# Kernel optimization log

Hardware: AMD Instinct MI355X
Metric: run time of the kernel (lower is better)

The kernel has to match this reference:

```python
import jax, jax.numpy as jnp
import numpy as np

B, T, E, NH, NLEV = 16, 2048, 1024, 16, 12
HD = E // NH


def _level_matrix(length):
    # Vectorized version of get_level_index_weak (base=2): levels[t, s] for s < t.
    tt, ss = np.meshgrid(np.arange(length), np.arange(length), indexing='ij')
    t = tt.copy(); s = ss.copy()
    lev = np.zeros((length, length), dtype=np.int32)
    active = tt > ss
    while active.any():
        l = np.floor(np.log2(np.maximum(t, 1))).astype(np.int64)
        v = (1 << l)
        done = active & (s < v)
        lev[done] = (l[done] + 1).astype(np.int32)
        cont = active & ~done
        t = np.where(cont, t - v, t)
        s = np.where(cont, s - v, s)
        active = cont
    return lev  # lev[t,t] = 0 (diagonal uses level 0)


def setup_inputs() -> dict:
    key = jax.random.key(0)
    ks = jax.random.split(key, 12)
    s = 0.02
    inp = {
        'x': jax.random.normal(ks[0], (B, T, E), jnp.float32),
        'Wq': jax.random.normal(ks[1], (E, E), jnp.float32) * s,
        'bq': jnp.zeros((E,), jnp.float32),
        'Wk': jax.random.normal(ks[2], (E, E), jnp.float32) * s,
        'bk': jnp.zeros((E,), jnp.float32),
        'Wv': jax.random.normal(ks[3], (E, E), jnp.float32) * s,
        'bv': jnp.zeros((E,), jnp.float32),
        'A_log': jax.random.normal(ks[4], (T, NH), jnp.float32),
        'A_bias': jnp.zeros((T, NH), jnp.float32),
        'L': jax.random.normal(ks[5], (T, NH, NLEV), jnp.float32),
        'L_bias': jnp.zeros((T, NH, NLEV), jnp.float32),
        'Wo': jax.random.normal(ks[6], (E, E), jnp.float32) * s,
        'bo': jnp.zeros((E,), jnp.float32),
        'levels': jnp.asarray(_level_matrix(T)),
    }
    return inp


def reference(x, Wq, bq, Wk, bk, Wv, bv, A_log, A_bias, L, L_bias, Wo, bo, levels):
    Bn, Tn, En = x.shape
    NHh = A_log.shape[1]
    HDd = En // NHh
    # q/k projections exist in the original forward but are never used by the
    # hierarchical attention; keep only v (q/k are dead code -> omitted).
    v = (x @ Wv.T + bv).reshape(Bn, Tn, NHh, HDd).transpose(0, 2, 1, 3)  # [B,H,T,D]

    # Decay factors: prod(A[s+1:t+1]) == exp(cumsum(logA)[t] - cumsum(logA)[s]).
    A = jax.nn.sigmoid(A_log + A_bias)            # [T, H]
    cs = jnp.cumsum(jnp.log(A), axis=0)           # [T, H]
    decay = jnp.exp(cs[:, None, :] - cs[None, :, :])  # [t, s, H]; diag == 1

    # Hierarchical level weights: G[t, s, h] = (L + L_bias)[t, h, levels[t, s]].
    Le = L + L_bias                               # [T, H, NLEV]
    G = Le[jnp.arange(Tn)[:, None], :, levels]    # [t, s, H]

    causal = jnp.tril(jnp.ones((Tn, Tn), dtype=bool))[:, :, None]
    Hm = jnp.where(causal, G * decay, jnp.zeros((), x.dtype))  # [t, s, H]

    # Original softmaxes the full row (upper triangle is 0, not -inf) -> keep that.
    attn = jax.nn.softmax(Hm, axis=1)             # over source dim s
    out = jnp.einsum('tsh,bhsd->bhtd', attn, v)   # [B,H,T,D]
    out = out.transpose(0, 2, 1, 3).reshape(Bn, Tn, En)
    return out @ Wo.T + bo
```

## Files before the change

kernel.cpp:

```cpp
#include <hip/hip_runtime.h>
#include <stdint.h>

static constexpr int Bn = 16, Tn = 2048, En = 1024, NHn = 16, HDn = 64, NLEVn = 12;

typedef __attribute__((ext_vector_type(8))) short short8;
typedef __attribute__((ext_vector_type(4))) float floatx4;

__device__ __forceinline__ unsigned short f2bf(float f) {
  unsigned int u = __float_as_uint(f);
  u += 0x7fffu + ((u >> 16) & 1u);
  return (unsigned short)(u >> 16);
}
__device__ __forceinline__ float bf2f(unsigned short s) {
  return __uint_as_float(((unsigned int)s) << 16);
}

__device__ __forceinline__ void async16(const unsigned short* g, unsigned short* l) {
  __builtin_amdgcn_global_load_lds(
      (const __attribute__((address_space(1))) unsigned int*)g,
      (__attribute__((address_space(3))) unsigned int*)l, 16, 0, 0);
}

__global__ void k_cvt(const float* __restrict__ in, unsigned short* __restrict__ out, int n4) {
  int i = blockIdx.x * 256 + threadIdx.x;
  if (i < n4) {
    float4 v = ((const float4*)in)[i];
    ushort4 o;
    o.x = f2bf(v.x); o.y = f2bf(v.y); o.z = f2bf(v.z); o.w = f2bf(v.w);
    ((ushort4*)out)[i] = o;
  }
}

__global__ void k_scan(const float* __restrict__ A_log, const float* __restrict__ A_bias,
                       float* __restrict__ csT) {
  int h = blockIdx.x;
  int tid = threadIdx.x;
  __shared__ float part[256];
  float loc[8];
  float run = 0.f;
#pragma unroll
  for (int j = 0; j < 8; j++) {
    int t = tid * 8 + j;
    float x = A_log[t * NHn + h] + A_bias[t * NHn + h];
    float ls = -log1pf(__expf(-x));
    run += ls;
    loc[j] = run;
  }
  part[tid] = run;
  __syncthreads();
  for (int d = 1; d < 256; d <<= 1) {
    float v = (tid >= d) ? part[tid - d] : 0.f;
    __syncthreads();
    part[tid] += v;
    __syncthreads();
  }
  float off = (tid > 0) ? part[tid - 1] : 0.f;
#pragma unroll
  for (int j = 0; j < 8; j++) csT[(size_t)h * Tn + tid * 8 + j] = loc[j] + off;
}

__global__ void k_weights(const float* __restrict__ L, const float* __restrict__ Lb,
                          const int* __restrict__ levels, const float* __restrict__ csT,
                          unsigned short* __restrict__ P, float* __restrict__ denom) {
  int t = blockIdx.x;
  int tid = threadIdx.x;
  __shared__ float Lrow[NHn * NLEVn];
  __shared__ float cst[NHn];
  __shared__ float dsum[NHn];
  if (tid < NHn * NLEVn) Lrow[tid] = L[t * NHn * NLEVn + tid] + Lb[t * NHn * NLEVn + tid];
  if (tid < NHn) { cst[tid] = csT[(size_t)tid * Tn + t]; dsum[tid] = 0.f; }
  __syncthreads();
  float acc[NHn];
#pragma unroll
  for (int h = 0; h < NHn; h++) acc[h] = 0.f;
  for (int s = tid; s < Tn; s += 256) {
    int lev = levels[(size_t)t * Tn + s];
    bool causal = (s <= t);
#pragma unroll
    for (int h = 0; h < NHn; h++) {
      float w = 1.f;
      if (causal) {
        float csr = csT[(size_t)h * Tn + s];
        float dec = __expf(cst[h] - csr);
        w = __expf(Lrow[h * NLEVn + lev] * dec);
      }
      unsigned short pb = f2bf(w);
      acc[h] += bf2f(pb);
      P[((size_t)h * Tn + t) * Tn + s] = pb;
    }
  }
  int lane = tid & 63;
#pragma unroll
  for (int h = 0; h < NHn; h++) {
    float v = acc[h];
    for (int o = 32; o > 0; o >>= 1) v += __shfl_down(v, o, 64);
    if (lane == 0) atomicAdd(&dsum[h], v);
  }
  __syncthreads();
  if (tid < NHn) denom[(size_t)tid * Tn + t] = dsum[tid];
}

__global__ __launch_bounds__(512)
void k_gemm_v(const unsigned short* __restrict__ A, const unsigned short* __restrict__ Bm,
              const float* __restrict__ bias, unsigned short* __restrict__ vt) {
  __shared__ unsigned short smem[24576];
  unsigned short* As = smem;
  unsigned short* Bs = smem + 16384;
  const int K = 1024;
  int tid = threadIdx.x;
  int wave = tid >> 6, lane = tid & 63;
  int wm = wave >> 1, wn = wave & 1;

  int flat = blockIdx.y * 8 + blockIdx.x;
  int xcd = flat & 7, slot = flat >> 3;
  int strip = xcd * 16 + (slot >> 3);
  int nt = slot & 7;
  int bm = strip * 256, bn = nt * 128;

  floatx4 zero4 = {0.f, 0.f, 0.f, 0.f};
  floatx4 acc[4][4];
#pragma unroll
  for (int i = 0; i < 4; i++)
#pragma unroll
    for (int j = 0; j < 4; j++) acc[i][j] = zero4;

  for (int k0 = 0; k0 < K; k0 += 64) {
    __syncthreads();
#pragma unroll
    for (int j = 0; j < 4; j++) {
      int f = j * 512 + tid;
      int r = f >> 3, c = f & 7;
      int cg = c ^ (r & 7);
      async16(&A[(size_t)(bm + r) * K + k0 + cg * 8], &As[f * 8]);
    }
#pragma unroll
    for (int j = 0; j < 2; j++) {
      int f = j * 512 + tid;
      int r = f >> 3, c = f & 7;
      int cg = c ^ (r & 7);
      async16(&Bm[(size_t)(bn + r) * K + k0 + cg * 8], &Bs[f * 8]);
    }
    __syncthreads();
#pragma unroll
    for (int kk = 0; kk < 2; kk++) {
      short8 af[4], bfr[4];
      int cgk = kk * 4 + (lane >> 4);
#pragma unroll
      for (int i = 0; i < 4; i++) {
        int m = wm * 64 + i * 16 + (lane & 15);
        af[i] = *(const short8*)&As[m * 64 + ((cgk ^ (m & 7)) * 8)];
        int n = wn * 64 + i * 16 + (lane & 15);
        bfr[i] = *(const short8*)&Bs[n * 64 + ((cgk ^ (n & 7)) * 8)];
      }
#pragma unroll
      for (int i = 0; i < 4; i++)
#pragma unroll
        for (int j = 0; j < 4; j++)
          acc[i][j] = __builtin_amdgcn_mfma_f32_16x16x32_bf16(af[i], bfr[j], acc[i][j], 0, 0, 0);
    }
  }

  int b = bm >> 11, t0 = bm & 2047;
  unsigned short* Ct = smem;
  const int S = 264;
#pragma unroll 1
  for (int pass = 0; pass < 2; pass++) {
    __syncthreads();
    if (wn == pass) {
#pragma unroll
      for (int i = 0; i < 4; i++) {
#pragma unroll
        for (int j = 0; j < 4; j++) {
          int colL = j * 16 + (lane & 15);
          float bia = bias[bn + pass * 64 + colL];
          int rowb = wm * 64 + i * 16 + (lane >> 4) * 4;
          ushort4 p;
          p.x = f2bf(acc[i][j][0] + bia);
          p.y = f2bf(acc[i][j][1] + bia);
          p.z = f2bf(acc[i][j][2] + bia);
          p.w = f2bf(acc[i][j][3] + bia);
          *(ushort4*)&Ct[colL * S + rowb] = p;
        }
      }
    }
    __syncthreads();
#pragma unroll
    for (int cc = 0; cc < 4; cc++) {
      int colL = wave * 8 + cc * 2 + (lane >> 5);
      int gc = bn + pass * 64 + colL;
      int h = gc >> 6, d = gc & 63;
      int tt = (lane & 31) * 8;
      short8 v = *(const short8*)&Ct[colL * S + tt];
      *(short8*)&vt[((size_t)((h * Bn + b) * HDn + d)) * Tn + t0 + tt] = v;
    }
  }
}


#define STAGE_A(kt, half, buf)                                                   \
  {                                                                              \
    _Pragma("unroll")                                                            \
    for (int j_ = 0; j_ < 2; j_++) {                                             \
      int f_ = j_ * 512 + tid;                                                   \
      int r_ = f_ >> 3, c_ = f_ & 7;                                             \
      int cg_ = c_ ^ (r_ & 7);                                                   \
      async16(&Ap[(size_t)(bm + (half) * 128 + r_) * K + (kt) * 64 + cg_ * 8],   \
              &smem[(buf) * 32768 + ((half) * 128 + r_) * 64 + c_ * 8]);         \
    }                                                                            \
  }

#define STAGE_B(kt, half, buf)                                                   \
  {                                                                              \
    _Pragma("unroll")                                                            \
    for (int j_ = 0; j_ < 2; j_++) {                                             \
      int f_ = j_ * 512 + tid;                                                   \
      int r_ = f_ >> 3, c_ = f_ & 7;                                             \
      int cg_ = c_ ^ (r_ & 7);                                                   \
      async16(&Bp[(size_t)(bn + (half) * 128 + r_) * K + (kt) * 64 + cg_ * 8],   \
              &smem[(buf) * 32768 + 16384 + ((half) * 128 + r_) * 64 + c_ * 8]); \
    }                                                                            \
  }

#define LOAD_A(buf, Mh)                                                          \
  {                                                                              \
    _Pragma("unroll")                                                            \
    for (int ii_ = 0; ii_ < 4; ii_++) {                                          \
      int m_ = (Mh) * 128 + wm * 64 + ii_ * 16 + (lane & 15);                    \
      _Pragma("unroll")                                                          \
      for (int kk_ = 0; kk_ < 2; kk_++) {                                        \
        int cgk_ = kk_ * 4 + (lane >> 4);                                        \
        aR[ii_][kk_] =                                                           \
            *(const short8*)&smem[(buf) * 32768 + m_ * 64 + ((cgk_ ^ (m_ & 7)) * 8)]; \
      }                                                                          \
    }                                                                            \
  }

#define LOAD_B(buf, Nh)                                                          \
  {                                                                              \
    _Pragma("unroll")                                                            \
    for (int jj_ = 0; jj_ < 2; jj_++) {                                          \
      int n_ = (Nh) * 128 + wn * 32 + jj_ * 16 + (lane & 15);                    \
      _Pragma("unroll")                                                          \
      for (int kk_ = 0; kk_ < 2; kk_++) {                                        \
        int cgk_ = kk_ * 4 + (lane >> 4);                                        \
        bR[jj_][kk_] = *(const short8*)&smem[(buf) * 32768 + 16384 + n_ * 64 +   \
                                             ((cgk_ ^ (n_ & 7)) * 8)];           \
      }                                                                          \
    }                                                                            \
  }

#define MFMA16(Mh, Nh)                                                           \
  {                                                                              \
    __builtin_amdgcn_s_setprio(1);                                               \
    _Pragma("unroll")                                                            \
    for (int kk_ = 0; kk_ < 2; kk_++)                                            \
      _Pragma("unroll")                                                          \
      for (int ii_ = 0; ii_ < 4; ii_++)                                          \
        _Pragma("unroll")                                                        \
        for (int jj_ = 0; jj_ < 2; jj_++)                                        \
          acc[(Mh) * 4 + ii_][(Nh) * 2 + jj_] = __builtin_amdgcn_mfma_f32_16x16x32_bf16( \
              aR[ii_][kk_], bR[jj_][kk_], acc[(Mh) * 4 + ii_][(Nh) * 2 + jj_], 0, 0, 0); \
    __builtin_amdgcn_s_setprio(0);                                               \
  }

#define WAIT6 asm volatile("s_waitcnt vmcnt(6)" ::: "memory")
#define BAR                                                                      \
  {                                                                              \
    asm volatile("" ::: "memory");                                               \
    __builtin_amdgcn_s_barrier();                                                \
    asm volatile("" ::: "memory");                                               \
  }

#define KTILE_BODY(buf, nbuf, tn)                                                \
  {                                                                              \
                                  \
    STAGE_A(tn, 0, nbuf);                                                        \
    WAIT6; BAR;                                                                  \
    LOAD_A(buf, 0);                                                              \
    LOAD_B(buf, 0);                                                              \
    MFMA16(0, 0);                                                                \
    BAR;                                                                         \
                               \
    STAGE_B(tn, 0, nbuf);                                                        \
    WAIT6; BAR;                                                                  \
    LOAD_B(buf, 1);                                                              \
    MFMA16(0, 1);                                                                \
    BAR;                                                                         \
                               \
    STAGE_B(tn, 1, nbuf);                                                        \
    WAIT6; BAR;                                                                  \
    LOAD_A(buf, 1);                                                              \
    MFMA16(1, 1);                                                                \
    BAR;                                                                         \
                            \
    STAGE_A(tn, 1, nbuf);                                                        \
    WAIT6; BAR;                                                                  \
    LOAD_B(buf, 0);                                                              \
    MFMA16(1, 0);                                                                \
    BAR;                                                                         \
  }

__global__ __launch_bounds__(512, 2)
void k_gemm_attn(const unsigned short* __restrict__ P, const unsigned short* __restrict__ vt,
                 const float* __restrict__ denom, unsigned short* __restrict__ outp) {
  __shared__ unsigned short smem[65536];
  const int K = Tn;
  int tid = threadIdx.x;
  int wave = tid >> 6, lane = tid & 63;
  int wm = wave >> 2, wn = wave & 3;

  int flat = blockIdx.y * 8 + blockIdx.x;
  int wg = (flat & 7) * 64 + (flat >> 3);
  int h = wg >> 5;
  int mt = (wg >> 2) & 7, nt = wg & 3;
  int bm = mt * 256, bn = nt * 256;

  const unsigned short* Ap = P + (size_t)h * Tn * Tn;
  const unsigned short* Bp = vt + (size_t)h * (Bn * HDn) * Tn;

  floatx4 zero4 = {0.f, 0.f, 0.f, 0.f};
  floatx4 acc[8][4];
#pragma unroll
  for (int i = 0; i < 8; i++)
#pragma unroll
    for (int j = 0; j < 4; j++) acc[i][j] = zero4;

  short8 aR[4][2], bR[2][2];

  STAGE_A(0, 0, 0);
  STAGE_B(0, 0, 0);
  STAGE_B(0, 1, 0);
  STAGE_A(0, 1, 0);

  const int nk = K / 64;
  for (int t = 0; t < nk; t++) {
    int buf = t & 1, nbuf = buf ^ 1;
    int tn = (t < nk - 1) ? t + 1 : nk - 1;
    KTILE_BODY(buf, nbuf, tn);
  }
  asm volatile("s_waitcnt vmcnt(0)" ::: "memory");

#pragma unroll
  for (int i = 0; i < 8; i++) {
    int rb = bm + (i >> 2) * 128 + wm * 64 + (i & 3) * 16 + (lane >> 4) * 4;
#pragma unroll
    for (int r = 0; r < 4; r++) {
      int row = rb + r;
      float sc = 1.f / denom[(size_t)h * Tn + row];
#pragma unroll
      for (int j = 0; j < 4; j++) {
        int col = bn + (j >> 1) * 128 + wn * 32 + (j & 1) * 16 + (lane & 15);
        int b = col >> 6, d = col & 63;
        outp[((size_t)(b * Tn + row)) * En + h * HDn + d] = f2bf(acc[i][j][r] * sc);
      }
    }
  }
}

__global__ __launch_bounds__(512, 2)
void k_gemm_out(const unsigned short* __restrict__ A, const unsigned short* __restrict__ Bm,
                const float* __restrict__ bias, float* __restrict__ out) {
  __shared__ unsigned short smem[65536];
  const int K = 1024, N = 1024;
  int tid = threadIdx.x;
  int wave = tid >> 6, lane = tid & 63;
  int wm = wave >> 2, wn = wave & 3;

  int flat = blockIdx.y * 8 + blockIdx.x;
  int wg = (flat & 7) * 64 + (flat >> 3);
  int mt = wg >> 2, nt = wg & 3;
  int bm = mt * 256, bn = nt * 256;

  const unsigned short* Ap = A;
  const unsigned short* Bp = Bm;

  floatx4 zero4 = {0.f, 0.f, 0.f, 0.f};
  floatx4 acc[8][4];
#pragma unroll
  for (int i = 0; i < 8; i++)
#pragma unroll
    for (int j = 0; j < 4; j++) acc[i][j] = zero4;

  short8 aR[4][2], bR[2][2];

  STAGE_A(0, 0, 0);
  STAGE_B(0, 0, 0);
  STAGE_B(0, 1, 0);
  STAGE_A(0, 1, 0);

  const int nk = K / 64;
  for (int t = 0; t < nk; t++) {
    int buf = t & 1, nbuf = buf ^ 1;
    int tn = (t < nk - 1) ? t + 1 : nk - 1;
    KTILE_BODY(buf, nbuf, tn);
  }
  asm volatile("s_waitcnt vmcnt(0)" ::: "memory");

#pragma unroll
  for (int i = 0; i < 8; i++) {
    int rb = bm + (i >> 2) * 128 + wm * 64 + (i & 3) * 16 + (lane >> 4) * 4;
#pragma unroll
    for (int r = 0; r < 4; r++) {
      int row = rb + r;
#pragma unroll
      for (int j = 0; j < 4; j++) {
        int col = bn + (j >> 1) * 128 + wn * 32 + (j & 1) * 16 + (lane & 15);
        out[(size_t)row * N + col] = acc[i][j][r] + bias[col];
      }
    }
  }
}

extern "C" void kernel_launch(void* const* d_in, const int* in_sizes, int n_in,
                              void* d_out, int out_size, void* d_ws, size_t ws_size,
                              hipStream_t stream) {
  const float* x      = (const float*)d_in[0];
  const float* Wv     = (const float*)d_in[5];
  const float* bv     = (const float*)d_in[6];
  const float* A_log  = (const float*)d_in[7];
  const float* A_bias = (const float*)d_in[8];
  const float* L      = (const float*)d_in[9];
  const float* Lb     = (const float*)d_in[10];
  const float* Wo     = (const float*)d_in[11];
  const float* bo     = (const float*)d_in[12];
  const int* levels   = (const int*)d_in[13];
  float* out = (float*)d_out;

  char* ws = (char*)d_ws;
  float* csT           = (float*)(ws + 0);
  float* denom         = (float*)(ws + 131072);
  unsigned short* Wvb  = (unsigned short*)(ws + 262144);
  unsigned short* Wob  = (unsigned short*)(ws + 2359296);
  unsigned short* xb   = (unsigned short*)(ws + 4456448);
  unsigned short* Pw   = (unsigned short*)(ws + 4456448);
  unsigned short* vt   = (unsigned short*)(ws + 138674176);
  unsigned short* outp = (unsigned short*)(ws + 205783040);
  if (ws_size < 272891904ULL) return;

  int nx4 = Bn * Tn * En / 4;
  k_cvt<<<(nx4 + 255) / 256, 256, 0, stream>>>(x, xb, nx4);
  int nw4 = En * En / 4;
  k_cvt<<<(nw4 + 255) / 256, 256, 0, stream>>>(Wv, Wvb, nw4);
  k_cvt<<<(nw4 + 255) / 256, 256, 0, stream>>>(Wo, Wob, nw4);
  k_scan<<<NHn, 256, 0, stream>>>(A_log, A_bias, csT);

  k_gemm_v<<<dim3(8, 128), 512, 0, stream>>>(xb, Wvb, bv, vt);

  k_weights<<<Tn, 256, 0, stream>>>(L, Lb, levels, csT, Pw, denom);

  k_gemm_attn<<<dim3(8, 64), 512, 0, stream>>>(Pw, vt, denom, outp);

  k_gemm_out<<<dim3(8, 64), 512, 0, stream>>>(outp, Wob, bo, out);
}
```

Before: 606.3 us.

## Skip upper-triangle blocks in attention GEMM using precomputed V tail sums

Past the causal diagonal every attention weight is exp(0)=1, so the weights kernel now writes only up to the 256-aligned block boundary and adds the constant tail count to the denominator. A new kernel precomputes suffix sums of V over 256-row blocks, and the attention GEMM runs K only up to its row tile, then adds the tail sum before normalising. This roughly halves the P writes and the attention GEMM work, at the cost of an extra small kernel. The tail sums are kept in scratch space at the end of the output buffer, which is overwritten later by the final GEMM.

After: 572.8 us. 1.06x faster.

```diff
diff --git a/kernel.cpp b/kernel.cpp
--- a/kernel.cpp
+++ b/kernel.cpp
@@ -70,10 +70,11 @@
   if (tid < NHn * NLEVn) Lrow[tid] = L[t * NHn * NLEVn + tid] + Lb[t * NHn * NLEVn + tid];
   if (tid < NHn) { cst[tid] = csT[(size_t)tid * Tn + t]; dsum[tid] = 0.f; }
   __syncthreads();
+  int Bt = ((t >> 8) + 1) << 8;
   float acc[NHn];
 #pragma unroll
   for (int h = 0; h < NHn; h++) acc[h] = 0.f;
-  for (int s = tid; s < Tn; s += 256) {
+  for (int s = tid; s < Bt; s += 256) {
     int lev = levels[(size_t)t * Tn + s];
     bool causal = (s <= t);
 #pragma unroll
@@ -97,7 +98,27 @@
     if (lane == 0) atomicAdd(&dsum[h], v);
   }
   __syncthreads();
-  if (tid < NHn) denom[(size_t)tid * Tn + t] = dsum[tid];
+  if (tid < NHn) denom[(size_t)tid * Tn + t] = dsum[tid] + (float)(Tn - Bt);
+}
+
+__global__ void k_tail(const unsigned short* __restrict__ vt, float* __restrict__ Stail) {
+  int row = blockIdx.x;
+  int tid = threadIdx.x;
+  __shared__ float C[8];
+  short8 v = *(const short8*)&vt[(size_t)row * Tn + tid * 8];
+  float p = 0.f;
+#pragma unroll
+  for (int e = 0; e < 8; e++) p += bf2f((unsigned short)v[e]);
+#pragma unroll
+  for (int o = 16; o > 0; o >>= 1) p += __shfl_xor(p, o, 64);
+  if ((tid & 31) == 0) C[tid >> 5] = p;
+  __syncthreads();
+  if (tid < 8) {
+    float s = 0.f;
+    for (int k = tid + 1; k < 8; k++) s += C[k];
+    int h = row >> 10, col = row & 1023;
+    Stail[(size_t)h * 8192 + tid * 1024 + col] = s;
+  }
 }
 
 __global__ __launch_bounds__(512)
@@ -302,7 +323,8 @@
 
 __global__ __launch_bounds__(512, 2)
 void k_gemm_attn(const unsigned short* __restrict__ P, const unsigned short* __restrict__ vt,
-                 const float* __restrict__ denom, unsigned short* __restrict__ outp) {
+                 const float* __restrict__ denom, const float* __restrict__ Stail,
+                 unsigned short* __restrict__ outp) {
   __shared__ unsigned short smem[65536];
   const int K = Tn;
   int tid = threadIdx.x;
@@ -332,13 +354,20 @@
   STAGE_B(0, 1, 0);
   STAGE_A(0, 1, 0);
 
-  const int nk = K / 64;
-  for (int t = 0; t < nk; t++) {
+  const int nkb = 4 * (mt + 1);
+  for (int t = 0; t < nkb; t++) {
     int buf = t & 1, nbuf = buf ^ 1;
-    int tn = (t < nk - 1) ? t + 1 : nk - 1;
+    int tn = (t < nkb - 1) ? t + 1 : nkb - 1;
     KTILE_BODY(buf, nbuf, tn);
   }
   asm volatile("s_waitcnt vmcnt(0)" ::: "memory");
+
+  float tl[4];
+#pragma unroll
+  for (int j = 0; j < 4; j++) {
+    int col = bn + (j >> 1) * 128 + wn * 32 + (j & 1) * 16 + (lane & 15);
+    tl[j] = Stail[(size_t)h * 8192 + mt * 1024 + col];
+  }
 
 #pragma unroll
   for (int i = 0; i < 8; i++) {
@@ -351,7 +380,7 @@
       for (int j = 0; j < 4; j++) {
         int col = bn + (j >> 1) * 128 + wn * 32 + (j & 1) * 16 + (lane & 15);
         int b = col >> 6, d = col & 63;
-        outp[((size_t)(b * Tn + row)) * En + h * HDn + d] = f2bf(acc[i][j][r] * sc);
+        outp[((size_t)(b * Tn + row)) * En + h * HDn + d] = f2bf((acc[i][j][r] + tl[j]) * sc);
       }
     }
   }
@@ -437,6 +466,8 @@
   unsigned short* outp = (unsigned short*)(ws + 205783040);
   if (ws_size < 272891904ULL) return;
 
+  float* Stail = out + (33554432 - 131072);
+
   int nx4 = Bn * Tn * En / 4;
   k_cvt<<<(nx4 + 255) / 256, 256, 0, stream>>>(x, xb, nx4);
   int nw4 = En * En / 4;
@@ -446,9 +477,11 @@
 
   k_gemm_v<<<dim3(8, 128), 512, 0, stream>>>(xb, Wvb, bv, vt);
 
+  k_tail<<<NHn * 1024, 256, 0, stream>>>(vt, Stail);
+
   k_weights<<<Tn, 256, 0, stream>>>(L, Lb, levels, csT, Pw, denom);
 
-  k_gemm_attn<<<dim3(8, 64), 512, 0, stream>>>(Pw, vt, denom, outp);
+  k_gemm_attn<<<dim3(8, 64), 512, 0, stream>>>(Pw, vt, denom, Stail, outp);
 
   k_gemm_out<<<dim3(8, 64), 512, 0, stream>>>(outp, Wob, bo, out);
 }
```
